# Performance work log

Measured on AMD Instinct MI355X. Metric: run time of the kernel, lower is better.

Reference implementation:

```python
import jax, jax.numpy as jnp
import numpy as np

B, D_IN, H1, H2, OUT = 8, 1024, 2048, 1024, 5120

def setup_inputs() -> dict:
    key = jax.random.key(0)
    ks = jax.random.split(key, 5)
    s1 = (6.0 / (D_IN + H1)) ** 0.5  # xavier_uniform-like scale
    s2 = (6.0 / (H1 + H2)) ** 0.5
    s3 = (6.0 / (H2 + OUT)) ** 0.5
    return {
        "x": jax.random.normal(ks[0], (B, D_IN), dtype=jnp.float32),
        "W1": jax.random.uniform(ks[1], (D_IN, H1), jnp.float32, -s1, s1),
        "b1": jnp.zeros((H1,), jnp.float32),
        "W2": jax.random.uniform(ks[2], (H1, H2), jnp.float32, -s2, s2),
        "b2": jnp.zeros((H2,), jnp.float32),
        "W3": jax.random.uniform(ks[3], (H2, OUT), jnp.float32, -s3, s3),
        "b3": jnp.zeros((OUT,), jnp.float32),
        "CM": jax.random.uniform(ks[4], (OUT, OUT), jnp.float32),
    }

def reference(x, W1, b1, W2, b2, W3, b3, CM):
    # MLP stack (eval mode: dropout is identity)
    h = jax.nn.relu(x @ W1 + b1)
    h = jax.nn.relu(h @ W2 + b2)
    features = h
    logits = h @ W3 + b3                      # [B, OUT]
    # tropical-style correlation: max_k logits[b,k] * CM[o,k]
    out = jnp.max(logits[:, None, :] * CM[None, :, :], axis=-1)  # [B, OUT]
    return out.astype(jnp.float32), features
```

## Files before the change

kernel.cpp:

```cpp
#include <hip/hip_runtime.h>
#include <cstdint>

#define B8   8
#define DIN  1024
#define NH1  2048
#define NH2  1024
#define NOUT 5120

__device__ __forceinline__ float4 ld4(const float* p) {
  return *reinterpret_cast<const float4*>(p);
}
__device__ __forceinline__ void st4(float* p, float4 v) {
  *reinterpret_cast<float4*>(p) = v;
}

template<int K, int N, int KSPLIT, int NPART, bool RELU_IN, bool WRITE_STAGE>
__global__ __launch_bounds__(256)
void gemm8(const float* __restrict__ Asrc, const float* __restrict__ bias_in,
           const float* __restrict__ W, float* __restrict__ Cparts,
           float* __restrict__ stage_out)
{
  constexpr int KC    = K / KSPLIT;
  constexpr int KC4   = KC / 4;
  constexpr int NCOLB = N / 64;
  constexpr int KT    = KC / 16;

  __shared__ float A_lds[8][KC];
  __shared__ float red[16][8][64];

  const int tid = threadIdx.x;
  const int kb  = blockIdx.x / NCOLB;
  const int cb  = blockIdx.x % NCOLB;
  const int k0  = kb * KC;

  for (int e = tid; e < 8 * KC4; e += 256) {
    const int b = e / KC4, k4 = e - b * KC4;
    float4 v;
    if constexpr (NPART == 0) {
      v = ld4(&Asrc[(size_t)b * K + k0 + 4 * k4]);
    } else {
      v = ld4(&bias_in[k0 + 4 * k4]);
      #pragma unroll
      for (int p = 0; p < NPART; ++p) {
        float4 t = ld4(&Asrc[((size_t)p * 8 + b) * K + k0 + 4 * k4]);
        v.x += t.x; v.y += t.y; v.z += t.z; v.w += t.w;
      }
      if constexpr (RELU_IN) {
        v.x = fmaxf(v.x, 0.f); v.y = fmaxf(v.y, 0.f);
        v.z = fmaxf(v.z, 0.f); v.w = fmaxf(v.w, 0.f);
      }
    }
    st4(&A_lds[b][4 * k4], v);
    if constexpr (WRITE_STAGE) {
      if (cb == 0) st4(&stage_out[(size_t)b * K + k0 + 4 * k4], v);
    }
  }
  __syncthreads();

  const int g  = tid & 15, ks = tid >> 4;
  const int c0 = cb * 64 + g * 4;
  float4 acc[8];
  #pragma unroll
  for (int b = 0; b < 8; ++b) acc[b] = make_float4(0.f, 0.f, 0.f, 0.f);

  const float* Wp = &W[(size_t)(k0 + ks * KT) * N + c0];
  #pragma unroll
  for (int i = 0; i < KT; i += 4) {
    const float4 w0 = ld4(Wp + (size_t)(i + 0) * N);
    const float4 w1 = ld4(Wp + (size_t)(i + 1) * N);
    const float4 w2 = ld4(Wp + (size_t)(i + 2) * N);
    const float4 w3 = ld4(Wp + (size_t)(i + 3) * N);
    const int kk = ks * KT + i;
    #pragma unroll
    for (int b = 0; b < 8; ++b) {
      const float4 a = ld4(&A_lds[b][kk]);
      acc[b].x += a.x * w0.x + a.y * w1.x + a.z * w2.x + a.w * w3.x;
      acc[b].y += a.x * w0.y + a.y * w1.y + a.z * w2.y + a.w * w3.y;
      acc[b].z += a.x * w0.z + a.y * w1.z + a.z * w2.z + a.w * w3.z;
      acc[b].w += a.x * w0.w + a.y * w1.w + a.z * w2.w + a.w * w3.w;
    }
  }

  __syncthreads();
  #pragma unroll
  for (int b = 0; b < 8; ++b) st4(&red[ks][b][g * 4], acc[b]);
  __syncthreads();

  for (int p = tid; p < 512; p += 256) {
    const int c = p & 63, b = p >> 6;
    float s = 0.f;
    #pragma unroll
    for (int j = 0; j < 16; ++j) s += red[j][b][c];
    Cparts[((size_t)kb * 8 + b) * N + cb * 64 + c] = s;
  }
}

__global__ __launch_bounds__(256)
void finalize_logits(const float* __restrict__ parts, const float* __restrict__ b3,
                     float* __restrict__ logits)
{
  const int i  = blockIdx.x * 256 + threadIdx.x;
  const int b  = i / 1280, k4 = i - b * 1280;
  float4 v = ld4(&b3[4 * k4]);
  #pragma unroll
  for (int p = 0; p < 4; ++p) {
    const float4 t = ld4(&parts[((size_t)p * 8 + b) * NOUT + 4 * k4]);
    v.x += t.x; v.y += t.y; v.z += t.z; v.w += t.w;
  }
  st4(&logits[(size_t)b * NOUT + 4 * k4], v);
}

__global__ __launch_bounds__(256)
void tropical(const float* __restrict__ logits, const float* __restrict__ CM,
              float* __restrict__ out)
{
  __shared__ float L[8][1024];

  const int tid = threadIdx.x;
  const int w   = tid >> 6;
  const int l   = tid & 63;
  const int ob0 = blockIdx.x * 16;

  float pmax[4][8];
  #pragma unroll
  for (int r = 0; r < 4; ++r)
    #pragma unroll
    for (int b = 0; b < 8; ++b) pmax[r][b] = -3.402823466e38f;

  for (int ck = 0; ck < NOUT; ck += 1024) {
    for (int e = tid; e < 2048; e += 256) {
      const int b = e >> 8, k4 = e & 255;
      st4(&L[b][4 * k4], ld4(&logits[(size_t)b * NOUT + ck + 4 * k4]));
    }
    __syncthreads();

    #pragma unroll
    for (int r = 0; r < 4; ++r) {
      const int o = ob0 + w * 4 + r;
      const float* cmrow = &CM[(size_t)o * NOUT + ck];
      #pragma unroll
      for (int i = 0; i < 4; ++i) {
        const int kk = 4 * (l + 64 * i);
        const float4 cm = ld4(&cmrow[kk]);
        #pragma unroll
        for (int b = 0; b < 8; ++b) {
          const float4 lv = ld4(&L[b][kk]);
          const float m0 = fmaxf(lv.x * cm.x, lv.y * cm.y);
          const float m1 = fmaxf(lv.z * cm.z, lv.w * cm.w);
          pmax[r][b] = fmaxf(pmax[r][b], fmaxf(m0, m1));
        }
      }
    }
    __syncthreads();
  }

  #pragma unroll
  for (int r = 0; r < 4; ++r) {
    #pragma unroll
    for (int b = 0; b < 8; ++b) {
      float v = pmax[r][b];
      for (int m = 32; m; m >>= 1) v = fmaxf(v, __shfl_xor(v, m));
      if (l == 0) out[(size_t)b * NOUT + ob0 + w * 4 + r] = v;
    }
  }
}

extern "C" void kernel_launch(void* const* d_in, const int* in_sizes, int n_in,
                              void* d_out, int out_size, void* d_ws, size_t ws_size,
                              hipStream_t stream)
{
  const float* x  = (const float*)d_in[0];
  const float* W1 = (const float*)d_in[1];
  const float* b1 = (const float*)d_in[2];
  const float* W2 = (const float*)d_in[3];
  const float* b2 = (const float*)d_in[4];
  const float* W3 = (const float*)d_in[5];
  const float* b3 = (const float*)d_in[6];
  const float* CM = (const float*)d_in[7];

  float* out  = (float*)d_out;
  float* feat = out + B8 * NOUT;

  float* ws     = (float*)d_ws;
  float* parts1 = ws;
  float* parts2 = parts1 + 8  * 8 * NH1;
  float* parts3 = parts2 + 16 * 8 * NH2;
  float* logits = parts3 + 4  * 8 * NOUT;

  gemm8<DIN, NH1, 8, 0, false, false><<<256, 256, 0, stream>>>(x, nullptr, W1, parts1, nullptr);
  gemm8<NH1, NH2, 16, 8, true, false><<<256, 256, 0, stream>>>(parts1, b1, W2, parts2, nullptr);
  gemm8<NH2, NOUT, 4, 16, true, true><<<320, 256, 0, stream>>>(parts2, b2, W3, parts3, feat);
  finalize_logits<<<40, 256, 0, stream>>>(parts3, b3, logits);
  tropical<<<320, 256, 0, stream>>>(logits, CM, out);
}
```

Measured before the change: 56.17 us.

## Split tropical max-product over K into parallel blocks with combine kernel

```diff
diff --git a/kernel.cpp b/kernel.cpp
--- a/kernel.cpp
+++ b/kernel.cpp
@@ -6,6 +6,7 @@
 #define NH1  2048
 #define NH2  1024
 #define NOUT 5120
+#define TKSPLIT 5
 
 __device__ __forceinline__ float4 ld4(const float* p) {
   return *reinterpret_cast<const float4*>(p);
@@ -111,15 +112,24 @@
 }
 
 __global__ __launch_bounds__(256)
-void tropical(const float* __restrict__ logits, const float* __restrict__ CM,
-              float* __restrict__ out)
+void tropical_part(const float* __restrict__ logits, const float* __restrict__ CM,
+                   float* __restrict__ partial)
 {
   __shared__ float L[8][1024];
 
   const int tid = threadIdx.x;
   const int w   = tid >> 6;
   const int l   = tid & 63;
-  const int ob0 = blockIdx.x * 16;
+  const int rg  = blockIdx.x / TKSPLIT;
+  const int ks  = blockIdx.x % TKSPLIT;
+  const int k0  = ks * 1024;
+  const int o0  = rg * 16 + w * 4;
+
+  for (int e = tid; e < 2048; e += 256) {
+    const int b = e >> 8, k4 = e & 255;
+    st4(&L[b][4 * k4], ld4(&logits[(size_t)b * NOUT + k0 + 4 * k4]));
+  }
+  __syncthreads();
 
   float pmax[4][8];
   #pragma unroll
@@ -127,31 +137,23 @@
     #pragma unroll
     for (int b = 0; b < 8; ++b) pmax[r][b] = -3.402823466e38f;
 
-  for (int ck = 0; ck < NOUT; ck += 1024) {
-    for (int e = tid; e < 2048; e += 256) {
-      const int b = e >> 8, k4 = e & 255;
-      st4(&L[b][4 * k4], ld4(&logits[(size_t)b * NOUT + ck + 4 * k4]));
-    }
-    __syncthreads();
-
-    #pragma unroll
-    for (int r = 0; r < 4; ++r) {
-      const int o = ob0 + w * 4 + r;
-      const float* cmrow = &CM[(size_t)o * NOUT + ck];
+  #pragma unroll
+  for (int i = 0; i < 4; ++i) {
+    const int kk = 4 * (l + 64 * i);
+    float4 cm[4];
+    #pragma unroll
+    for (int r = 0; r < 4; ++r)
+      cm[r] = ld4(&CM[(size_t)(o0 + r) * NOUT + k0 + kk]);
+    #pragma unroll
+    for (int b = 0; b < 8; ++b) {
+      const float4 lv = ld4(&L[b][kk]);
       #pragma unroll
-      for (int i = 0; i < 4; ++i) {
-        const int kk = 4 * (l + 64 * i);
-        const float4 cm = ld4(&cmrow[kk]);
-        #pragma unroll
-        for (int b = 0; b < 8; ++b) {
-          const float4 lv = ld4(&L[b][kk]);
-          const float m0 = fmaxf(lv.x * cm.x, lv.y * cm.y);
-          const float m1 = fmaxf(lv.z * cm.z, lv.w * cm.w);
-          pmax[r][b] = fmaxf(pmax[r][b], fmaxf(m0, m1));
-        }
+      for (int r = 0; r < 4; ++r) {
+        const float m0 = fmaxf(lv.x * cm[r].x, lv.y * cm[r].y);
+        const float m1 = fmaxf(lv.z * cm[r].z, lv.w * cm[r].w);
+        pmax[r][b] = fmaxf(pmax[r][b], fmaxf(m0, m1));
       }
     }
-    __syncthreads();
   }
 
   #pragma unroll
@@ -160,9 +162,23 @@
     for (int b = 0; b < 8; ++b) {
       float v = pmax[r][b];
       for (int m = 32; m; m >>= 1) v = fmaxf(v, __shfl_xor(v, m));
-      if (l == 0) out[(size_t)b * NOUT + ob0 + w * 4 + r] = v;
-    }
-  }
+      if (l == 0) partial[((size_t)ks * 8 + b) * NOUT + o0 + r] = v;
+    }
+  }
+}
+
+__global__ __launch_bounds__(256)
+void tropical_combine(const float* __restrict__ partial, float* __restrict__ out)
+{
+  const int i = blockIdx.x * 256 + threadIdx.x;
+  float4 v = ld4(&partial[4 * (size_t)i]);
+  #pragma unroll
+  for (int p = 1; p < TKSPLIT; ++p) {
+    const float4 t = ld4(&partial[(size_t)p * 8 * NOUT + 4 * (size_t)i]);
+    v.x = fmaxf(v.x, t.x); v.y = fmaxf(v.y, t.y);
+    v.z = fmaxf(v.z, t.z); v.w = fmaxf(v.w, t.w);
+  }
+  st4(&out[4 * (size_t)i], v);
 }
 
 extern "C" void kernel_launch(void* const* d_in, const int* in_sizes, int n_in,
@@ -181,15 +197,17 @@
   float* out  = (float*)d_out;
   float* feat = out + B8 * NOUT;
 
-  float* ws     = (float*)d_ws;
-  float* parts1 = ws;
-  float* parts2 = parts1 + 8  * 8 * NH1;
-  float* parts3 = parts2 + 16 * 8 * NH2;
-  float* logits = parts3 + 4  * 8 * NOUT;
+  float* ws      = (float*)d_ws;
+  float* parts1  = ws;
+  float* parts2  = parts1 + 8  * 8 * NH1;
+  float* parts3  = parts2 + 16 * 8 * NH2;
+  float* logits  = parts3 + 4  * 8 * NOUT;
+  float* tpart   = logits + 8 * NOUT;
 
   gemm8<DIN, NH1, 8, 0, false, false><<<256, 256, 0, stream>>>(x, nullptr, W1, parts1, nullptr);
   gemm8<NH1, NH2, 16, 8, true, false><<<256, 256, 0, stream>>>(parts1, b1, W2, parts2, nullptr);
   gemm8<NH2, NOUT, 4, 16, true, true><<<320, 256, 0, stream>>>(parts2, b2, W3, parts3, feat);
   finalize_logits<<<40, 256, 0, stream>>>(parts3, b3, logits);
-  tropical<<<320, 256, 0, stream>>>(logits, CM, out);
-}
+  tropical_part<<<1600, 256, 0, stream>>>(logits, CM, tpart);
+  tropical_combine<<<40, 256, 0, stream>>>(tpart, out);
+}
```

Result: slower. 71.21 us (+26.8%).
